# Optimization experiments

Hardware: AMD Instinct MI355X
Metric: run time of the kernel (lower is better)

The kernel has to match this reference:

```python
import jax, jax.numpy as jnp
import numpy as np
import math

D_MODEL = 1024
NUM_HEADS = 16
NUM_LAYERS = 4
D_FF = 4096
TEXT_DIM = 512
B, SV, ST = 4, 2048, 100
EPS = 1e-5


def positional_encoding(seq_len, d):
    pos = jnp.arange(seq_len, dtype=jnp.float32)[:, None]
    div = jnp.exp(jnp.arange(0, d, 2, dtype=jnp.float32) * (-math.log(10000.0) / d))
    pe = jnp.zeros((seq_len, d), dtype=jnp.float32)
    pe = pe.at[:, 0::2].set(jnp.sin(pos * div))
    pe = pe.at[:, 1::2].set(jnp.cos(pos * div))
    return pe  # [seq_len, d]


def layer_norm(x, g, b):
    mu = jnp.mean(x, axis=-1, keepdims=True)
    var = jnp.mean(jnp.square(x - mu), axis=-1, keepdims=True)
    return (x - mu) * jax.lax.rsqrt(var + EPS) * g + b


def setup_inputs() -> dict:
    key = jax.random.key(0)
    ks = jax.random.split(key, 24)
    s = 0.02
    inp = {
        "video": jax.random.normal(ks[0], (B, SV, D_MODEL), jnp.float32),
        "text": jax.random.normal(ks[1], (B, ST, TEXT_DIM), jnp.float32),
        "text_mask": jnp.ones((B, ST), jnp.int32),
        # stacked per-layer params, weights stored [in, out]
        "Wq_w": jax.random.normal(ks[2], (NUM_LAYERS, D_MODEL, D_MODEL)) * s,
        "Wq_b": jnp.zeros((NUM_LAYERS, D_MODEL)),
        "Wk_w": jax.random.normal(ks[3], (NUM_LAYERS, TEXT_DIM, D_MODEL)) * s,
        "Wk_b": jnp.zeros((NUM_LAYERS, D_MODEL)),
        "Wv_w": jax.random.normal(ks[4], (NUM_LAYERS, TEXT_DIM, D_MODEL)) * s,
        "Wv_b": jnp.zeros((NUM_LAYERS, D_MODEL)),
        "Wo_w": jax.random.normal(ks[5], (NUM_LAYERS, D_MODEL, D_MODEL)) * s,
        "Wo_b": jnp.zeros((NUM_LAYERS, D_MODEL)),
        "fc1_w": jax.random.normal(ks[6], (NUM_LAYERS, D_MODEL, D_FF)) * s,
        "fc1_b": jnp.zeros((NUM_LAYERS, D_FF)),
        "fc2_w": jax.random.normal(ks[7], (NUM_LAYERS, D_FF, D_MODEL)) * s,
        "fc2_b": jnp.zeros((NUM_LAYERS, D_MODEL)),
        "n2_g": jnp.ones((NUM_LAYERS, D_MODEL)),
        "n2_b": jnp.zeros((NUM_LAYERS, D_MODEL)),
        "n3_g": jnp.ones((NUM_LAYERS, D_MODEL)),
        "n3_b": jnp.zeros((NUM_LAYERS, D_MODEL)),
    }
    return inp


def cross_attn_layer(video, text, mask, wq, bq, wk, bk, wv, bv, wo, bo):
    Bv, Sq, D = video.shape
    H, dk = NUM_HEADS, D_MODEL // NUM_HEADS
    q = (video @ wq + bq).reshape(Bv, Sq, H, dk).transpose(0, 2, 1, 3)  # bhqd
    k = (text @ wk + bk).reshape(Bv, -1, H, dk).transpose(0, 2, 1, 3)   # bhkd
    v = (text @ wv + bv).reshape(Bv, -1, H, dk).transpose(0, 2, 1, 3)
    scores = jnp.einsum("bhqd,bhkd->bhqk", q, k) / math.sqrt(dk)
    scores = jnp.where(mask, scores, jnp.float32(-1e9))
    probs = jax.nn.softmax(scores, axis=-1)
    out = jnp.einsum("bhqk,bhkd->bhqd", probs, v)
    out = out.transpose(0, 2, 1, 3).reshape(Bv, Sq, D)
    return out @ wo + bo


def reference(video, text, text_mask, Wq_w, Wq_b, Wk_w, Wk_b, Wv_w, Wv_b,
              Wo_w, Wo_b, fc1_w, fc1_b, fc2_w, fc2_b, n2_g, n2_b, n3_g, n3_b):
    video = video + positional_encoding(SV, D_MODEL)[None, :video.shape[1]]
    text = text + positional_encoding(ST, TEXT_DIM)[None, :text.shape[1]]
    mask = (text_mask != 0)[:, None, None, :]  # [B,1,1,St]
    for l in range(NUM_LAYERS):
        attn = cross_attn_layer(video, text, mask,
                                Wq_w[l], Wq_b[l], Wk_w[l], Wk_b[l],
                                Wv_w[l], Wv_b[l], Wo_w[l], Wo_b[l])
        video = layer_norm(video + attn, n2_g[l], n2_b[l])
        ff = jax.nn.relu(video @ fc1_w[l] + fc1_b[l]) @ fc2_w[l] + fc2_b[l]
        video = layer_norm(video + ff, n3_g[l], n3_b[l])
    return video
```

## Files before the change

### kernel.cpp

```cpp
#include <hip/hip_runtime.h>
#include <cstdint>
#include <cstddef>

typedef unsigned short u16;
typedef __attribute__((ext_vector_type(8))) __bf16 bf16x8;
typedef __attribute__((ext_vector_type(4))) float f32x4;

__device__ __forceinline__ f32x4 mfma_16x16x32(bf16x8 a, bf16x8 b, f32x4 c) {
  return __builtin_amdgcn_mfma_f32_16x16x32_bf16(a, b, c, 0, 0, 0);
}

__device__ __forceinline__ u16 f2bf(float f) {
  union { float f; uint32_t u; } c; c.f = f;
  uint32_t u = c.u + 0x7FFFu + ((c.u >> 16) & 1u);
  return (u16)(u >> 16);
}

__device__ __forceinline__ float bf2f(u16 x) {
  union { uint32_t u; float f; } c; c.u = ((uint32_t)x) << 16;
  return c.f;
}

__device__ __forceinline__ void gload_lds16(const void* g, void* l) {
  __builtin_amdgcn_global_load_lds(
      (__attribute__((address_space(1))) void*)(uintptr_t)g,
      (__attribute__((address_space(3))) void*)l, 16, 0, 0);
}

template<int MR, bool OUT_BF16, bool RELU, bool ACC>
__global__ __launch_bounds__(512, 2) void gemm_ring(
    const u16* __restrict__ A, int lda, const u16* __restrict__ Bt, int ldb,
    const float* __restrict__ bias, void* Cout, int ldc,
    int M, int N, int K)
{
  constexpr int BM = MR * 32;
  constexpr int SLOT = (BM + 256) * 32;
  __shared__ u16 ring[4 * SLOT];

  const int tid = threadIdx.x;
  const int lane = tid & 63, wave = tid >> 6;
  const int wm = wave >> 2, wn = wave & 3;
  const int m0 = blockIdx.x * BM, n0 = blockIdx.y * 256;

  const int cA0 = tid, rA0 = cA0 >> 2;
  const u16* gA0 = A + (size_t)(m0 + rA0) * lda + (((cA0 & 3) ^ ((rA0 >> 1) & 3)) * 8);
  const int cA1 = tid + 512, rA1 = cA1 >> 2;
  const u16* gA1 = A + (size_t)(m0 + (MR == 8 ? rA1 : 0)) * lda + (((cA1 & 3) ^ ((rA1 >> 1) & 3)) * 8);
  const int cB0 = tid, rB0 = cB0 >> 2;
  const int cB1 = tid + 512, rB1 = cB1 >> 2;
  const u16* gB0 = Bt + (size_t)(n0 + rB0) * ldb + (((cB0 & 3) ^ ((rB0 >> 1) & 3)) * 8);
  const u16* gB1 = Bt + (size_t)(n0 + rB1) * ldb + (((cB1 & 3) ^ ((rB1 >> 1) & 3)) * 8);

  const int NK = K >> 5;

  auto STAGE = [&](int s) {
    u16* Sb = &ring[(s & 3) * SLOT];
    const int ko = s * 32;
    gload_lds16(gA0 + ko, Sb + cA0 * 8);
    if constexpr (MR == 8) gload_lds16(gA1 + ko, Sb + cA1 * 8);
    gload_lds16(gB0 + ko, Sb + BM * 32 + cB0 * 8);
    gload_lds16(gB1 + ko, Sb + BM * 32 + cB1 * 8);
  };
  auto WAITV = [&](int ahead) {
    if (ahead >= 2) {
      if constexpr (MR == 8) asm volatile("s_waitcnt vmcnt(8)" ::: "memory");
      else                   asm volatile("s_waitcnt vmcnt(6)" ::: "memory");
    } else if (ahead == 1) {
      if constexpr (MR == 8) asm volatile("s_waitcnt vmcnt(4)" ::: "memory");
      else                   asm volatile("s_waitcnt vmcnt(3)" ::: "memory");
    } else {
      asm volatile("s_waitcnt vmcnt(0)" ::: "memory");
    }
  };

  const int fr = lane & 15, g = lane >> 4;
  const int foff = fr * 32 + ((g ^ ((fr >> 1) & 3)) * 8);

  f32x4 acc[MR][4];
  #pragma unroll
  for (int m = 0; m < MR; m++)
    #pragma unroll
    for (int n = 0; n < 4; n++) acc[m][n] = f32x4{0.f, 0.f, 0.f, 0.f};

  for (int i = 0; i < 3 && i < NK; ++i) STAGE(i);
  WAITV(NK - 1 < 2 ? NK - 1 : 2);
  __builtin_amdgcn_s_barrier();
  __builtin_amdgcn_sched_barrier(0);

  for (int s = 0; s < NK; ++s) {
    const u16* As = &ring[(s & 3) * SLOT];
    const u16* Bs = As + BM * 32;

    bf16x8 bf[4];
    #pragma unroll
    for (int n = 0; n < 4; n++)
      bf[n] = *(const bf16x8*)(Bs + (wn * 64 + n * 16) * 32 + foff);
    bf16x8 af[4];
    #pragma unroll
    for (int m = 0; m < 4; m++)
      af[m] = *(const bf16x8*)(As + (wm * (MR * 16) + m * 16) * 32 + foff);

    if (s + 3 < NK) STAGE(s + 3);

    __builtin_amdgcn_s_setprio(1);
    #pragma unroll
    for (int m = 0; m < 4; m++)
      #pragma unroll
      for (int n = 0; n < 4; n++)
        acc[m][n] = mfma_16x16x32(af[m], bf[n], acc[m][n]);
    __builtin_amdgcn_s_setprio(0);

    if constexpr (MR == 8) {
      bf16x8 af2[4];
      #pragma unroll
      for (int m = 0; m < 4; m++)
        af2[m] = *(const bf16x8*)(As + (wm * 128 + (m + 4) * 16) * 32 + foff);
      __builtin_amdgcn_s_setprio(1);
      #pragma unroll
      for (int m = 0; m < 4; m++)
        #pragma unroll
        for (int n = 0; n < 4; n++)
          acc[m + 4][n] = mfma_16x16x32(af2[m], bf[n], acc[m + 4][n]);
      __builtin_amdgcn_s_setprio(0);
    }

    {
      int im = (s + 3 < NK - 1) ? s + 3 : NK - 1;
      WAITV(im - (s + 1));
    }
    asm volatile("s_waitcnt lgkmcnt(0)" ::: "memory");
    __builtin_amdgcn_sched_barrier(0);
    __builtin_amdgcn_s_barrier();
    __builtin_amdgcn_sched_barrier(0);
  }

  #pragma unroll
  for (int n = 0; n < 4; n++) {
    const int gcol = n0 + wn * 64 + n * 16 + fr;
    const float bv = bias ? bias[gcol] : 0.f;
    #pragma unroll
    for (int m = 0; m < MR; m++) {
      #pragma unroll
      for (int r = 0; r < 4; r++) {
        const int grow = m0 + wm * (MR * 16) + m * 16 + g * 4 + r;
        float v = acc[m][n][r] + bv;
        if (ACC) v += bf2f(((const u16*)Cout)[(size_t)grow * ldc + gcol]);
        if (RELU) v = fmaxf(v, 0.f);
        if (OUT_BF16) ((u16*)Cout)[(size_t)grow * ldc + gcol] = f2bf(v);
        else         ((float*)Cout)[(size_t)grow * ldc + gcol] = v;
      }
    }
  }
}

template<bool TRANS>
__global__ __launch_bounds__(256, 2) void gemm_bt(
    const u16* __restrict__ A, int lda, const u16* __restrict__ Bt, int ldb,
    const float* __restrict__ bias, u16* Cout, int ldc,
    int M, int N, int K)
{
  __shared__ u16 ldsA[128 * 32];
  __shared__ u16 ldsB[128 * 32];

  const int tid = threadIdx.x;
  const int lane = tid & 63, wave = tid >> 6;
  const int wr = wave >> 1, wc = wave & 1;
  const int m0 = blockIdx.x * 128, n0 = blockIdx.y * 128;

  const int c0 = tid, c1 = tid + 256;
  const int ar0 = c0 >> 2, ak0 = (c0 & 3) * 8;
  const int ar1 = c1 >> 2, ak1 = (c1 & 3) * 8;

  const bool av0 = (m0 + ar0) < M;
  const bool av1 = (m0 + ar1) < M;
  const u16* Ag0 = A + (size_t)(m0 + ar0) * lda + ak0;
  const u16* Ag1 = A + (size_t)(m0 + ar1) * lda + ak1;
  const u16* Bg0 = Bt + (size_t)(n0 + ar0) * ldb + ak0;
  const u16* Bg1 = Bt + (size_t)(n0 + ar1) * ldb + ak1;

  f32x4 acc[4][4] = {};
  const int fr = lane & 15, fo = (lane >> 4) * 8;

  for (int k0 = 0; k0 < K; k0 += 32) {
    if (av0) gload_lds16(Ag0 + k0, &ldsA[c0 * 8]);
    if (av1) gload_lds16(Ag1 + k0, &ldsA[c1 * 8]);
    gload_lds16(Bg0 + k0, &ldsB[c0 * 8]);
    gload_lds16(Bg1 + k0, &ldsB[c1 * 8]);
    asm volatile("s_waitcnt vmcnt(0)" ::: "memory");
    __syncthreads();

    bf16x8 af[4], bfr[4];
    #pragma unroll
    for (int m = 0; m < 4; m++)
      af[m] = *(const bf16x8*)&ldsA[(wr * 64 + m * 16 + fr) * 32 + fo];
    #pragma unroll
    for (int n = 0; n < 4; n++)
      bfr[n] = *(const bf16x8*)&ldsB[(wc * 64 + n * 16 + fr) * 32 + fo];
    #pragma unroll
    for (int m = 0; m < 4; m++)
      #pragma unroll
      for (int n = 0; n < 4; n++)
        acc[m][n] = mfma_16x16x32(af[m], bfr[n], acc[m][n]);
    __syncthreads();
  }

  const int g = lane >> 4;
  #pragma unroll
  for (int m = 0; m < 4; m++) {
    #pragma unroll
    for (int n = 0; n < 4; n++) {
      const int gcol = n0 + wc * 64 + n * 16 + fr;
      const float bv = bias[gcol];
      #pragma unroll
      for (int r = 0; r < 4; r++) {
        const int grow = m0 + wr * 64 + m * 16 + g * 4 + r;
        if (grow < M) {
          float v = acc[m][n][r] + bv;
          if (TRANS) {
            int bb = grow / 100, jj = grow - bb * 100;
            int h = gcol >> 6, d = gcol & 63;
            Cout[(size_t)(((bb * 16 + h) * 64 + d)) * 128 + jj] = f2bf(v);
          } else {
            Cout[(size_t)grow * ldc + gcol] = f2bf(v);
          }
        }
      }
    }
  }
}

__global__ void wconv_t(const float* __restrict__ src, u16* __restrict__ dst,
                        int K, int N)
{
  __shared__ float tile[32][33];
  const int n0 = blockIdx.x * 32, k0 = blockIdx.y * 32;
  const int tx = threadIdx.x, ty = threadIdx.y;
  #pragma unroll
  for (int i = 0; i < 4; i++)
    tile[ty + i * 8][tx] = src[(size_t)(k0 + ty + i * 8) * N + n0 + tx];
  __syncthreads();
  #pragma unroll
  for (int i = 0; i < 4; i++)
    dst[(size_t)(n0 + ty + i * 8) * K + k0 + tx] = f2bf(tile[tx][ty + i * 8]);
}

__global__ __launch_bounds__(256) void pe_video_k(const float* __restrict__ video,
                                                  u16* __restrict__ vbf)
{
  const int r = blockIdx.x;
  const int s = r & 2047;
  const int d0 = threadIdx.x * 4;
  const size_t base = (size_t)r * 1024 + d0;
  float4 v = *(const float4*)&video[base];
  const float coef = -9.210340371976184f / 1024.f;
  float o[4];
  float in[4] = {v.x, v.y, v.z, v.w};
  #pragma unroll
  for (int i = 0; i < 4; i++) {
    int d = d0 + i;
    int j = d >> 1;
    float dv = expf((float)(2 * j) * coef);
    float arg = (float)s * dv;
    float pe = (d & 1) ? cosf(arg) : sinf(arg);
    o[i] = in[i] + pe;
  }
  uint2 pk;
  pk.x = (uint32_t)f2bf(o[0]) | ((uint32_t)f2bf(o[1]) << 16);
  pk.y = (uint32_t)f2bf(o[2]) | ((uint32_t)f2bf(o[3]) << 16);
  *(uint2*)&vbf[base] = pk;
}

__global__ __launch_bounds__(128) void pe_text_k(const float* __restrict__ text,
                                                 u16* __restrict__ tbf)
{
  const int r = blockIdx.x;
  const int s = r % 100;
  const int d0 = threadIdx.x * 4;
  const size_t base = (size_t)r * 512 + d0;
  float4 v = *(const float4*)&text[base];
  const float coef = -9.210340371976184f / 512.f;
  float o[4];
  float in[4] = {v.x, v.y, v.z, v.w};
  #pragma unroll
  for (int i = 0; i < 4; i++) {
    int d = d0 + i;
    int j = d >> 1;
    float dv = expf((float)(2 * j) * coef);
    float arg = (float)s * dv;
    float pe = (d & 1) ? cosf(arg) : sinf(arg);
    o[i] = in[i] + pe;
  }
  uint2 pk;
  pk.x = (uint32_t)f2bf(o[0]) | ((uint32_t)f2bf(o[1]) << 16);
  pk.y = (uint32_t)f2bf(o[2]) | ((uint32_t)f2bf(o[3]) << 16);
  *(uint2*)&tbf[base] = pk;
}

template<bool LAST>
__global__ __launch_bounds__(256) void ln2(const u16* __restrict__ xin,
                                           const u16* __restrict__ delta,
                                           const float* __restrict__ gamma,
                                           const float* __restrict__ beta,
                                           u16* __restrict__ xbf,
                                           float* __restrict__ fout)
{
  const int row = blockIdx.x;
  const size_t base = (size_t)row * 1024;
  const int t = threadIdx.x;
  const int d0 = t * 4;
  uint2 xv = *(const uint2*)&xin[base + d0];
  uint2 dv = *(const uint2*)&delta[base + d0];
  float v0 = bf2f((u16)(xv.x & 0xFFFF)) + bf2f((u16)(dv.x & 0xFFFF));
  float v1 = bf2f((u16)(xv.x >> 16))    + bf2f((u16)(dv.x >> 16));
  float v2 = bf2f((u16)(xv.y & 0xFFFF)) + bf2f((u16)(dv.y & 0xFFFF));
  float v3 = bf2f((u16)(xv.y >> 16))    + bf2f((u16)(dv.y >> 16));
  float s = v0 + v1 + v2 + v3;
  float q = v0 * v0 + v1 * v1 + v2 * v2 + v3 * v3;
  #pragma unroll
  for (int d = 32; d >= 1; d >>= 1) { s += __shfl_xor(s, d); q += __shfl_xor(q, d); }
  __shared__ float red[8];
  const int lane = t & 63, w = t >> 6;
  if (lane == 0) { red[w] = s; red[4 + w] = q; }
  __syncthreads();
  float S = red[0] + red[1] + red[2] + red[3];
  float Qs = red[4] + red[5] + red[6] + red[7];
  const float mu = S * (1.f / 1024.f);
  const float var = Qs * (1.f / 1024.f) - mu * mu;
  const float rs = rsqrtf(var + 1e-5f);
  float4 gv = *(const float4*)&gamma[d0];
  float4 bv = *(const float4*)&beta[d0];
  float o0 = (v0 - mu) * rs * gv.x + bv.x;
  float o1 = (v1 - mu) * rs * gv.y + bv.y;
  float o2 = (v2 - mu) * rs * gv.z + bv.z;
  float o3 = (v3 - mu) * rs * gv.w + bv.w;
  if (LAST) {
    *(float4*)&fout[base + d0] = make_float4(o0, o1, o2, o3);
  } else {
    uint2 pk;
    pk.x = (uint32_t)f2bf(o0) | ((uint32_t)f2bf(o1) << 16);
    pk.y = (uint32_t)f2bf(o2) | ((uint32_t)f2bf(o3) << 16);
    *(uint2*)&xbf[base + d0] = pk;
  }
}

__global__ __launch_bounds__(256) void attn_v2(
    const u16* __restrict__ Q, const u16* __restrict__ Kb,
    const u16* __restrict__ Vtb, const int* __restrict__ mask,
    u16* __restrict__ Out)
{
  __shared__ u16 ldsP[64 * 136];

  const int tid = threadIdx.x, lane = tid & 63, w = tid >> 6;
  const int qb = blockIdx.x, bh = blockIdx.y;
  const int b = bh >> 4, h = bh & 15;
  const int fr = lane & 15, g = lane >> 4, fo = g * 8;

  const size_t qrow = (size_t)(b * 2048 + qb * 64 + w * 16 + fr) * 1024 + h * 64;
  bf16x8 qf0 = *(const bf16x8*)&Q[qrow + fo];
  bf16x8 qf1 = *(const bf16x8*)&Q[qrow + 32 + fo];

  float madd[7];
  #pragma unroll
  for (int t = 0; t < 7; t++) {
    int col = t * 16 + fr;
    int mv = (col < 100) ? mask[b * 100 + col] : 0;
    madd[t] = mv ? 0.f : -1e30f;
  }

  float sc[7][4];
  #pragma unroll
  for (int t = 0; t < 7; t++) {
    int col = t * 16 + fr;
    int jr = (col < 100) ? col : 99;
    const u16* kp = Kb + (size_t)(b * 100 + jr) * 1024 + h * 64;
    bf16x8 kf0 = *(const bf16x8*)&kp[fo];
    bf16x8 kf1 = *(const bf16x8*)&kp[32 + fo];
    f32x4 a = {};
    a = mfma_16x16x32(qf0, kf0, a);
    a = mfma_16x16x32(qf1, kf1, a);
    #pragma unroll
    for (int r = 0; r < 4; r++)
      sc[t][r] = a[r] * 0.125f + madd[t];
  }

  #pragma unroll
  for (int r = 0; r < 4; r++) {
    float m = sc[0][r];
    #pragma unroll
    for (int t = 1; t < 7; t++) m = fmaxf(m, sc[t][r]);
    #pragma unroll
    for (int d = 8; d >= 1; d >>= 1) m = fmaxf(m, __shfl_xor(m, d));
    float ssum = 0.f;
    #pragma unroll
    for (int t = 0; t < 7; t++) { float p = __expf(sc[t][r] - m); sc[t][r] = p; ssum += p; }
    #pragma unroll
    for (int d = 8; d >= 1; d >>= 1) ssum += __shfl_xor(ssum, d);
    float is = 1.f / ssum;
    #pragma unroll
    for (int t = 0; t < 7; t++)
      ldsP[(w * 16 + g * 4 + r) * 136 + t * 16 + fr] = f2bf(sc[t][r] * is);
  }
  {
    u16* zp = &ldsP[(w * 16 + fr) * 136 + 112 + g * 6];
    #pragma unroll
    for (int i = 0; i < 6; i++) zp[i] = 0;
  }

  bf16x8 pa[4];
  #pragma unroll
  for (int kk = 0; kk < 4; kk++)
    pa[kk] = *(const bf16x8*)&ldsP[(w * 16 + fr) * 136 + kk * 32 + fo];
  const u16* vtbase = Vtb + (size_t)bh * 64 * 128;
  #pragma unroll
  for (int nt = 0; nt < 4; nt++) {
    f32x4 a = {};
    #pragma unroll
    for (int kk = 0; kk < 4; kk++) {
      bf16x8 vf = *(const bf16x8*)&vtbase[(size_t)(nt * 16 + fr) * 128 + kk * 32 + fo];
      a = mfma_16x16x32(pa[kk], vf, a);
    }
    #pragma unroll
    for (int r = 0; r < 4; r++) {
      size_t orow = (size_t)(b * 2048 + qb * 64 + w * 16 + g * 4 + r) * 1024 + h * 64 + nt * 16 + fr;
      Out[orow] = f2bf(a[r]);
    }
  }
}

extern "C" void kernel_launch(void* const* d_in, const int* in_sizes, int n_in,
                              void* d_out, int out_size, void* d_ws, size_t ws_size,
                              hipStream_t stream) {
  const float* video = (const float*)d_in[0];
  const float* text  = (const float*)d_in[1];
  const int*   text_mask = (const int*)d_in[2];
  const float* Wq_w = (const float*)d_in[3];
  const float* Wq_b = (const float*)d_in[4];
  const float* Wk_w = (const float*)d_in[5];
  const float* Wk_b = (const float*)d_in[6];
  const float* Wv_w = (const float*)d_in[7];
  const float* Wv_b = (const float*)d_in[8];
  const float* Wo_w = (const float*)d_in[9];
  const float* Wo_b = (const float*)d_in[10];
  const float* fc1_w = (const float*)d_in[11];
  const float* fc1_b = (const float*)d_in[12];
  const float* fc2_w = (const float*)d_in[13];
  const float* fc2_b = (const float*)d_in[14];
  const float* n2_g = (const float*)d_in[15];
  const float* n2_b = (const float*)d_in[16];
  const float* n3_g = (const float*)d_in[17];
  const float* n3_b = (const float*)d_in[18];

  char* ws = (char*)d_ws;
  size_t off = 0;
  auto alloc = [&](size_t bytes) {
    char* p = ws + off;
    off += (bytes + 255) & ~(size_t)255;
    return p;
  };
  u16* vbf = (u16*)alloc((size_t)8192 * 1024 * 2);
  u16* tbf = (u16*)alloc((size_t)400 * 512 * 2);
  u16* wqT = (u16*)alloc((size_t)1024 * 1024 * 2);
  u16* wkT = (u16*)alloc((size_t)1024 * 512 * 2);
  u16* wvT = (u16*)alloc((size_t)1024 * 512 * 2);
  u16* woT = (u16*)alloc((size_t)1024 * 1024 * 2);
  u16* f1T = (u16*)alloc((size_t)4096 * 1024 * 2);
  u16* f2T = (u16*)alloc((size_t)1024 * 4096 * 2);
  char* S = alloc((size_t)35192832);
  u16* qbf  = (u16*)S;
  u16* kbf  = (u16*)(S + 16777216);
  u16* abf  = (u16*)(S + 16777216 + 1638400);
  u16* h1c  = (u16*)S;
  u16* vtb  = (u16*)alloc((size_t)64 * 64 * 128 * 2);
  u16* dbf  = (u16*)alloc((size_t)8192 * 1024 * 2);
  float* fout = (float*)d_out;

  hipMemsetAsync(vtb, 0, (size_t)64 * 64 * 128 * 2, stream);

  pe_video_k<<<8192, 256, 0, stream>>>(video, vbf);
  pe_text_k<<<400, 128, 0, stream>>>(text, tbf);

  dim3 tb(32, 8, 1);
  for (int l = 0; l < 4; ++l) {
    wconv_t<<<dim3(32, 32), tb, 0, stream>>>(Wq_w + (size_t)l * 1024 * 1024, wqT, 1024, 1024);
    wconv_t<<<dim3(32, 16), tb, 0, stream>>>(Wk_w + (size_t)l * 512 * 1024, wkT, 512, 1024);
    wconv_t<<<dim3(32, 16), tb, 0, stream>>>(Wv_w + (size_t)l * 512 * 1024, wvT, 512, 1024);
    wconv_t<<<dim3(32, 32), tb, 0, stream>>>(Wo_w + (size_t)l * 1024 * 1024, woT, 1024, 1024);
    wconv_t<<<dim3(128, 32), tb, 0, stream>>>(fc1_w + (size_t)l * 1024 * 4096, f1T, 1024, 4096);
    wconv_t<<<dim3(32, 128), tb, 0, stream>>>(fc2_w + (size_t)l * 4096 * 1024, f2T, 4096, 1024);

    gemm_ring<4, true, false, false><<<dim3(64, 4), 512, 0, stream>>>(
        vbf, 1024, wqT, 1024, Wq_b + l * 1024, qbf, 1024, 8192, 1024, 1024);
    gemm_bt<false><<<dim3(4, 8), 256, 0, stream>>>(
        tbf, 512, wkT, 512, Wk_b + l * 1024, kbf, 1024, 400, 1024, 512);
    gemm_bt<true><<<dim3(4, 8), 256, 0, stream>>>(
        tbf, 512, wvT, 512, Wv_b + l * 1024, vtb, 1024, 400, 1024, 512);
    attn_v2<<<dim3(32, 64), 256, 0, stream>>>(qbf, kbf, vtb, text_mask, abf);
    gemm_ring<4, true, false, false><<<dim3(64, 4), 512, 0, stream>>>(
        abf, 1024, woT, 1024, Wo_b + l * 1024, dbf, 1024, 8192, 1024, 1024);
    ln2<false><<<8192, 256, 0, stream>>>(vbf, dbf, n2_g + l * 1024, n2_b + l * 1024, vbf, nullptr);

    for (int c = 0; c < 2; ++c) {
      gemm_ring<8, true, true, false><<<dim3(32, 8), 512, 0, stream>>>(
          vbf, 1024, f1T + (size_t)c * 2048 * 1024, 1024,
          fc1_b + l * 4096 + c * 2048, h1c, 2048, 8192, 2048, 1024);
      if (c == 0)
        gemm_ring<4, true, false, false><<<dim3(64, 4), 512, 0, stream>>>(
            h1c, 2048, f2T + (size_t)c * 2048, 4096,
            fc2_b + l * 1024, dbf, 1024, 8192, 1024, 2048);
      else
        gemm_ring<4, true, false, true><<<dim3(64, 4), 512, 0, stream>>>(
            h1c, 2048, f2T + (size_t)c * 2048, 4096,
            nullptr, dbf, 1024, 8192, 1024, 2048);
    }
    if (l == 3)
      ln2<true><<<8192, 256, 0, stream>>>(vbf, dbf, n3_g + l * 1024, n3_b + l * 1024, nullptr, fout);
    else
      ln2<false><<<8192, 256, 0, stream>>>(vbf, dbf, n3_g + l * 1024, n3_b + l * 1024, vbf, nullptr);
  }
}
```

Measured before the change: 1.314 ms.

## Replace 512-thread GEMM ring with 256-thread 256x128 tile, 3-slot pipeline

Replaces the templated 8-wave GEMM, which used 128x256 or 256x256 tiles and a 4-deep LDS ring, with a single 4-wave kernel. Each wave computes a 128x64 output sub-tile using a 3-slot ring with prefetch distance two. Every GEMM launch gets new grid shapes to match the 256x128 tile. The aim is more MFMA work per LDS fragment load per wave and less LDS use per block, which may allow higher occupancy. The cost is a shallower prefetch and more accumulator registers per thread (128 floats).

```diff
diff --git a/kernel.cpp b/kernel.cpp
--- a/kernel.cpp
+++ b/kernel.cpp
@@ -27,111 +27,103 @@
       (__attribute__((address_space(3))) void*)l, 16, 0, 0);
 }
 
-template<int MR, bool OUT_BF16, bool RELU, bool ACC>
-__global__ __launch_bounds__(512, 2) void gemm_ring(
+template<bool OUT_BF16, bool RELU, bool ACC>
+__global__ __launch_bounds__(256, 2) void gemm_ring3(
     const u16* __restrict__ A, int lda, const u16* __restrict__ Bt, int ldb,
     const float* __restrict__ bias, void* Cout, int ldc,
     int M, int N, int K)
 {
-  constexpr int BM = MR * 32;
-  constexpr int SLOT = (BM + 256) * 32;
-  __shared__ u16 ring[4 * SLOT];
+  constexpr int BM = 256, BN = 128;
+  constexpr int SLOT = (BM + BN) * 32;
+  __shared__ u16 ring[3 * SLOT];
 
   const int tid = threadIdx.x;
   const int lane = tid & 63, wave = tid >> 6;
-  const int wm = wave >> 2, wn = wave & 3;
-  const int m0 = blockIdx.x * BM, n0 = blockIdx.y * 256;
-
-  const int cA0 = tid, rA0 = cA0 >> 2;
-  const u16* gA0 = A + (size_t)(m0 + rA0) * lda + (((cA0 & 3) ^ ((rA0 >> 1) & 3)) * 8);
-  const int cA1 = tid + 512, rA1 = cA1 >> 2;
-  const u16* gA1 = A + (size_t)(m0 + (MR == 8 ? rA1 : 0)) * lda + (((cA1 & 3) ^ ((rA1 >> 1) & 3)) * 8);
-  const int cB0 = tid, rB0 = cB0 >> 2;
-  const int cB1 = tid + 512, rB1 = cB1 >> 2;
-  const u16* gB0 = Bt + (size_t)(n0 + rB0) * ldb + (((cB0 & 3) ^ ((rB0 >> 1) & 3)) * 8);
-  const u16* gB1 = Bt + (size_t)(n0 + rB1) * ldb + (((cB1 & 3) ^ ((rB1 >> 1) & 3)) * 8);
+  const int wm = wave >> 1, wn = wave & 1;
+  const int m0 = blockIdx.x * BM, n0 = blockIdx.y * BN;
+
+  const u16* gA[4];
+  #pragma unroll
+  for (int i = 0; i < 4; i++) {
+    int c = tid + i * 256, r = c >> 2;
+    gA[i] = A + (size_t)(m0 + r) * lda + (((c & 3) ^ ((r >> 1) & 3)) * 8);
+  }
+  const u16* gB[2];
+  #pragma unroll
+  for (int i = 0; i < 2; i++) {
+    int c = tid + i * 256, r = c >> 2;
+    gB[i] = Bt + (size_t)(n0 + r) * ldb + (((c & 3) ^ ((r >> 1) & 3)) * 8);
+  }
 
   const int NK = K >> 5;
 
-  auto STAGE = [&](int s) {
-    u16* Sb = &ring[(s & 3) * SLOT];
+  auto STAGE = [&](int s, int ph) {
+    u16* Sb = &ring[ph * SLOT];
     const int ko = s * 32;
-    gload_lds16(gA0 + ko, Sb + cA0 * 8);
-    if constexpr (MR == 8) gload_lds16(gA1 + ko, Sb + cA1 * 8);
-    gload_lds16(gB0 + ko, Sb + BM * 32 + cB0 * 8);
-    gload_lds16(gB1 + ko, Sb + BM * 32 + cB1 * 8);
-  };
-  auto WAITV = [&](int ahead) {
-    if (ahead >= 2) {
-      if constexpr (MR == 8) asm volatile("s_waitcnt vmcnt(8)" ::: "memory");
-      else                   asm volatile("s_waitcnt vmcnt(6)" ::: "memory");
-    } else if (ahead == 1) {
-      if constexpr (MR == 8) asm volatile("s_waitcnt vmcnt(4)" ::: "memory");
-      else                   asm volatile("s_waitcnt vmcnt(3)" ::: "memory");
-    } else {
-      asm volatile("s_waitcnt vmcnt(0)" ::: "memory");
-    }
+    #pragma unroll
+    for (int i = 0; i < 4; i++)
+      gload_lds16(gA[i] + ko, Sb + (tid + i * 256) * 8);
+    #pragma unroll
+    for (int i = 0; i < 2; i++)
+      gload_lds16(gB[i] + ko, Sb + BM * 32 + (tid + i * 256) * 8);
   };
 
   const int fr = lane & 15, g = lane >> 4;
   const int foff = fr * 32 + ((g ^ ((fr >> 1) & 3)) * 8);
 
-  f32x4 acc[MR][4];
-  #pragma unroll
-  for (int m = 0; m < MR; m++)
+  f32x4 acc[8][4];
+  #pragma unroll
+  for (int m = 0; m < 8; m++)
     #pragma unroll
     for (int n = 0; n < 4; n++) acc[m][n] = f32x4{0.f, 0.f, 0.f, 0.f};
 
-  for (int i = 0; i < 3 && i < NK; ++i) STAGE(i);
-  WAITV(NK - 1 < 2 ? NK - 1 : 2);
+  STAGE(0, 0);
+  if (NK > 1) {
+    STAGE(1, 1);
+    asm volatile("s_waitcnt vmcnt(6)" ::: "memory");
+  } else {
+    asm volatile("s_waitcnt vmcnt(0)" ::: "memory");
+  }
   __builtin_amdgcn_s_barrier();
   __builtin_amdgcn_sched_barrier(0);
 
+  int phys = 0;
+  int physN = (NK > 1) ? 1 : 0;
   for (int s = 0; s < NK; ++s) {
-    const u16* As = &ring[(s & 3) * SLOT];
+    const u16* As = &ring[phys * SLOT];
     const u16* Bs = As + BM * 32;
 
     bf16x8 bf[4];
     #pragma unroll
     for (int n = 0; n < 4; n++)
       bf[n] = *(const bf16x8*)(Bs + (wn * 64 + n * 16) * 32 + foff);
-    bf16x8 af[4];
-    #pragma unroll
-    for (int m = 0; m < 4; m++)
-      af[m] = *(const bf16x8*)(As + (wm * (MR * 16) + m * 16) * 32 + foff);
-
-    if (s + 3 < NK) STAGE(s + 3);
+    bf16x8 af[8];
+    #pragma unroll
+    for (int m = 0; m < 8; m++)
+      af[m] = *(const bf16x8*)(As + (wm * 128 + m * 16) * 32 + foff);
+
+    if (s + 2 < NK) {
+      int ph2 = physN + 1 == 3 ? 0 : physN + 1;
+      STAGE(s + 2, ph2);
+      physN = ph2;
+    }
 
     __builtin_amdgcn_s_setprio(1);
     #pragma unroll
-    for (int m = 0; m < 4; m++)
+    for (int m = 0; m < 8; m++)
       #pragma unroll
       for (int n = 0; n < 4; n++)
         acc[m][n] = mfma_16x16x32(af[m], bf[n], acc[m][n]);
     __builtin_amdgcn_s_setprio(0);
 
-    if constexpr (MR == 8) {
-      bf16x8 af2[4];
-      #pragma unroll
-      for (int m = 0; m < 4; m++)
-        af2[m] = *(const bf16x8*)(As + (wm * 128 + (m + 4) * 16) * 32 + foff);
-      __builtin_amdgcn_s_setprio(1);
-      #pragma unroll
-      for (int m = 0; m < 4; m++)
-        #pragma unroll
-        for (int n = 0; n < 4; n++)
-          acc[m + 4][n] = mfma_16x16x32(af2[m], bf[n], acc[m + 4][n]);
-      __builtin_amdgcn_s_setprio(0);
-    }
-
-    {
-      int im = (s + 3 < NK - 1) ? s + 3 : NK - 1;
-      WAITV(im - (s + 1));
-    }
+    if (s + 2 < NK) asm volatile("s_waitcnt vmcnt(6)" ::: "memory");
+    else            asm volatile("s_waitcnt vmcnt(0)" ::: "memory");
     asm volatile("s_waitcnt lgkmcnt(0)" ::: "memory");
     __builtin_amdgcn_sched_barrier(0);
     __builtin_amdgcn_s_barrier();
     __builtin_amdgcn_sched_barrier(0);
+
+    phys = phys + 1 == 3 ? 0 : phys + 1;
   }
 
   #pragma unroll
@@ -139,10 +131,10 @@
     const int gcol = n0 + wn * 64 + n * 16 + fr;
     const float bv = bias ? bias[gcol] : 0.f;
     #pragma unroll
-    for (int m = 0; m < MR; m++) {
+    for (int m = 0; m < 8; m++) {
       #pragma unroll
       for (int r = 0; r < 4; r++) {
-        const int grow = m0 + wm * (MR * 16) + m * 16 + g * 4 + r;
+        const int grow = m0 + wm * 128 + m * 16 + g * 4 + r;
         float v = acc[m][n][r] + bv;
         if (ACC) v += bf2f(((const u16*)Cout)[(size_t)grow * ldc + gcol]);
         if (RELU) v = fmaxf(v, 0.f);
@@ -488,27 +480,27 @@
     wconv_t<<<dim3(128, 32), tb, 0, stream>>>(fc1_w + (size_t)l * 1024 * 4096, f1T, 1024, 4096);
     wconv_t<<<dim3(32, 128), tb, 0, stream>>>(fc2_w + (size_t)l * 4096 * 1024, f2T, 4096, 1024);
 
-    gemm_ring<4, true, false, false><<<dim3(64, 4), 512, 0, stream>>>(
+    gemm_ring3<true, false, false><<<dim3(32, 8), 256, 0, stream>>>(
         vbf, 1024, wqT, 1024, Wq_b + l * 1024, qbf, 1024, 8192, 1024, 1024);
     gemm_bt<false><<<dim3(4, 8), 256, 0, stream>>>(
         tbf, 512, wkT, 512, Wk_b + l * 1024, kbf, 1024, 400, 1024, 512);
     gemm_bt<true><<<dim3(4, 8), 256, 0, stream>>>(
         tbf, 512, wvT, 512, Wv_b + l * 1024, vtb, 1024, 400, 1024, 512);
     attn_v2<<<dim3(32, 64), 256, 0, stream>>>(qbf, kbf, vtb, text_mask, abf);
-    gemm_ring<4, true, false, false><<<dim3(64, 4), 512, 0, stream>>>(
+    gemm_ring3<true, false, false><<<dim3(32, 8), 256, 0, stream>>>(
         abf, 1024, woT, 1024, Wo_b + l * 1024, dbf, 1024, 8192, 1024, 1024);
     ln2<false><<<8192, 256, 0, stream>>>(vbf, dbf, n2_g + l * 1024, n2_b + l * 1024, vbf, nullptr);
 
     for (int c = 0; c < 2; ++c) {
-      gemm_ring<8, true, true, false><<<dim3(32, 8), 512, 0, stream>>>(
+      gemm_ring3<true, true, false><<<dim3(32, 16), 256, 0, stream>>>(
           vbf, 1024, f1T + (size_t)c * 2048 * 1024, 1024,
           fc1_b + l * 4096 + c * 2048, h1c, 2048, 8192, 2048, 1024);
       if (c == 0)
-        gemm_ring<4, true, false, false><<<dim3(64, 4), 512, 0, stream>>>(
+        gemm_ring3<true, false, false><<<dim3(32, 8), 256, 0, stream>>>(
             h1c, 2048, f2T + (size_t)c * 2048, 4096,
             fc2_b + l * 1024, dbf, 1024, 8192, 1024, 2048);
       else
-        gemm_ring<4, true, false, true><<<dim3(64, 4), 512, 0, stream>>>(
+        gemm_ring3<true, false, true><<<dim3(32, 8), 256, 0, stream>>>(
             h1c, 2048, f2T + (size_t)c * 2048, 4096,
             nullptr, dbf, 1024, 8192, 1024, 2048);
     }
```

Measured after the change: 1.396 ms. 1.06x slower.
